# Kernel tuning notes

Measured on AMD Instinct MI355X. Metric: run time of the kernel, lower is better.

Reference implementation:

```python
import jax, jax.numpy as jnp
import numpy as np

B, S, D_IN, D_OUT, H = 2, 2048, 1024, 1024, 16
HD = D_OUT // H  # 64


def setup_inputs() -> dict:
    key = jax.random.key(0)
    ks = jax.random.split(key, 6)
    s = 0.02
    return {
        "x": jax.random.normal(ks[0], (B, S, D_IN), dtype=jnp.float32),
        "W_q": jax.random.normal(ks[1], (D_IN, D_OUT), dtype=jnp.float32) * s,
        "W_k": jax.random.normal(ks[2], (D_IN, D_OUT), dtype=jnp.float32) * s,
        "W_v": jax.random.normal(ks[3], (D_IN, D_OUT), dtype=jnp.float32) * s,
        "W_o": jax.random.normal(ks[4], (D_OUT, D_OUT), dtype=jnp.float32) * s,
        "b_o": jax.random.normal(ks[5], (D_OUT,), dtype=jnp.float32) * s,
    }


def reference(x, W_q, W_k, W_v, W_o, b_o):
    b, n, _ = x.shape
    # project and split heads: [b, h, n, hd]
    q = (x @ W_q).reshape(b, n, H, HD).transpose(0, 2, 1, 3)
    k = (x @ W_k).reshape(b, n, H, HD).transpose(0, 2, 1, 3)
    v = (x @ W_v).reshape(b, n, H, HD).transpose(0, 2, 1, 3)
    scores = jnp.einsum("bhqd,bhkd->bhqk", q, k) / jnp.sqrt(jnp.float32(HD))
    causal = jnp.tril(jnp.ones((n, n), dtype=bool))
    scores = jnp.where(causal, scores, -jnp.inf)
    attn = jax.nn.softmax(scores, axis=-1)  # dropout p=0.0 -> identity
    ctx = jnp.einsum("bhqk,bhkd->bhqd", attn, v)
    ctx = ctx.transpose(0, 2, 1, 3).reshape(b, n, D_OUT)
    return ctx @ W_o + b_o
```

## Files before the change

kernel.cpp:

```cpp
#include <hip/hip_runtime.h>

#define B_    2
#define S_    2048
#define DIN   1024
#define DOUT  1024
#define H_    16
#define HD_   64
#define M_    (B_ * S_)

typedef __bf16 bf16x8 __attribute__((ext_vector_type(8)));
typedef float  f32x4  __attribute__((ext_vector_type(4)));

__device__ __forceinline__ f32x4 MFMA(bf16x8 a, bf16x8 b, f32x4 c) {
    return __builtin_amdgcn_mfma_f32_16x16x32_bf16(a, b, c, 0, 0, 0);
}

__device__ __forceinline__ unsigned short f2b(float f) {
    union { float f; unsigned int u; } v; v.f = f;
    unsigned int u = v.u;
    return (unsigned short)((u + 0x7fffu + ((u >> 16) & 1u)) >> 16);
}

__device__ __forceinline__ unsigned pack2(float a, float b) {
    union { __bf16 h[2]; unsigned u; } cv;
    cv.h[0] = (__bf16)a; cv.h[1] = (__bf16)b;
    return cv.u;
}

#define GLDS(gp, lp) __builtin_amdgcn_global_load_lds( \
    (const __attribute__((address_space(1))) void*)(gp), \
    (__attribute__((address_space(3))) void*)(lp), 16, 0, 0)

#define QSCALE 0.1803368801111204f

__global__ __launch_bounds__(256) void k_cvt_all(const float* __restrict__ x,
                                                 const float* __restrict__ Wq,
                                                 const float* __restrict__ Wk,
                                                 const float* __restrict__ Wv,
                                                 const float* __restrict__ Wo,
                                                 unsigned short* __restrict__ xb,
                                                 unsigned short* __restrict__ WqkvT,
                                                 unsigned short* __restrict__ WoT) {
    __shared__ __align__(16) float tile[64][68];
    int bid = blockIdx.x;
    int tid = threadIdx.x;
    if (bid < 1024) {
#pragma unroll
        for (int j = 0; j < 4; j++) {
            int i = bid * 4096 + j * 1024 + tid * 4;
            float4 v = *reinterpret_cast<const float4*>(x + i);
            ushort4 o;
            o.x = f2b(v.x); o.y = f2b(v.y); o.z = f2b(v.z); o.w = f2b(v.w);
            *reinterpret_cast<ushort4*>(xb + i) = o;
        }
        return;
    }
    int wb = bid - 1024;
    int w = wb >> 8;
    int t = wb & 255;
    const float* src = (w == 0) ? Wq : (w == 1) ? Wk : (w == 2) ? Wv : Wo;
    unsigned short* dst = (w < 3) ? WqkvT + (size_t)w * 1024 * DIN : WoT;
    int k0 = (t >> 4) * 64, n0 = (t & 15) * 64;
#pragma unroll
    for (int j = 0; j < 4; j++) {
        int idx = j * 256 + tid;
        int r = idx >> 4, c4 = (idx & 15) * 4;
        *reinterpret_cast<float4*>(&tile[r][c4]) =
            *reinterpret_cast<const float4*>(&src[(size_t)(k0 + r) * DOUT + n0 + c4]);
    }
    __syncthreads();
#pragma unroll
    for (int j = 0; j < 2; j++) {
        int idx = j * 256 + tid;
        int n = idx >> 3, gk = (idx & 7) * 8;
        unsigned short o[8];
#pragma unroll
        for (int u = 0; u < 8; u++) o[u] = f2b(tile[gk + u][n]);
        *reinterpret_cast<int4*>(&dst[(size_t)(n0 + n) * DIN + k0 + gk]) =
            *reinterpret_cast<int4*>(o);
    }
}

__global__ __launch_bounds__(256) void k_trV(const unsigned short* __restrict__ V,
                                             unsigned short* __restrict__ Vt) {
    __shared__ unsigned short tile[64][72];
    int st = blockIdx.x, bh = blockIdx.y;
    int b = bh >> 4, h = bh & 15;
    int t = threadIdx.x;
    int r = t >> 2, c = (t & 3) << 4;
    const unsigned short* src = V + (size_t)(b * S_ + st * 64 + r) * DOUT + h * HD_ + c;
    *reinterpret_cast<int4*>(&tile[r][c])     = *reinterpret_cast<const int4*>(src);
    *reinterpret_cast<int4*>(&tile[r][c + 8]) = *reinterpret_cast<const int4*>(src + 8);
    __syncthreads();
    unsigned short o[16];
    for (int j = 0; j < 16; j++) o[j] = tile[c + j][r];
    unsigned short* dst = Vt + (size_t)(bh * 64 + r) * S_ + st * 64 + c;
    *reinterpret_cast<int4*>(dst)     = *reinterpret_cast<int4*>(&o[0]);
    *reinterpret_cast<int4*>(dst + 8) = *reinterpret_cast<int4*>(&o[8]);
}

template <int OUT_MODE, int BM>
__global__ __launch_bounds__(256) void k_gemm(const unsigned short* __restrict__ A,
                                              const unsigned short* __restrict__ Bt,
                                              unsigned short* __restrict__ Cq,
                                              unsigned short* __restrict__ Ck,
                                              unsigned short* __restrict__ Cv,
                                              float* __restrict__ Cf,
                                              const float* __restrict__ bias,
                                              int M, int N, int K, int nbx) {
    constexpr int MI = BM / 32;
    __shared__ __align__(16) unsigned short As[BM * 64];
    __shared__ __align__(16) unsigned short Bs[128 * 64];

    int nwg = gridDim.x;
    int chunkw = nwg >> 3;
    int bid = blockIdx.x;
    int nid = (bid & 7) * chunkw + (bid >> 3);
    int by = nid / nbx, bx = nid - by * nbx;
    int m0 = by * BM, n0 = bx * 128;

    int tid = threadIdx.x;
    int wid = tid >> 6, lane = tid & 63;
    int wm = wid >> 1, wn = wid & 1;
    int lr = lane & 15, lg = lane >> 4;

    f32x4 acc[MI][4] = {};

    int srow = lane >> 3;
    int scol = ((lane & 7) ^ srow) * 8;
    int rsw  = lr & 7;

    for (int k0 = 0; k0 < K; k0 += 64) {
#pragma unroll
        for (int c = 0; c < MI; c++) {
            int chunk = wid * MI + c;
            int row = chunk * 8 + srow;
            GLDS(A + (size_t)(m0 + row) * K + k0 + scol, (char*)As + chunk * 1024);
        }
#pragma unroll
        for (int c = 0; c < 4; c++) {
            int chunk = wid * 4 + c;
            int row = chunk * 8 + srow;
            GLDS(Bt + (size_t)(n0 + row) * K + k0 + scol, (char*)Bs + chunk * 1024);
        }
        __syncthreads();

#pragma unroll
        for (int kk = 0; kk < 2; kk++) {
            bf16x8 af[MI], bf[4];
#pragma unroll
            for (int mi = 0; mi < MI; mi++)
                af[mi] = *reinterpret_cast<const bf16x8*>(
                    &As[(wm * (BM / 2) + mi * 16 + lr) * 64 + (((kk * 4 + lg) ^ rsw) * 8)]);
#pragma unroll
            for (int ni = 0; ni < 4; ni++)
                bf[ni] = *reinterpret_cast<const bf16x8*>(
                    &Bs[(wn * 64 + ni * 16 + lr) * 64 + (((kk * 4 + lg) ^ rsw) * 8)]);
#pragma unroll
            for (int mi = 0; mi < MI; mi++)
#pragma unroll
                for (int ni = 0; ni < 4; ni++)
                    acc[mi][ni] = MFMA(af[mi], bf[ni], acc[mi][ni]);
        }
        __syncthreads();
    }

    for (int mi = 0; mi < MI; mi++)
        for (int ni = 0; ni < 4; ni++)
            for (int i = 0; i < 4; i++) {
                int row = m0 + wm * (BM / 2) + mi * 16 + lg * 4 + i;
                int col = n0 + wn * 64 + ni * 16 + lr;
                float v = acc[mi][ni][i];
                if (OUT_MODE == 2) {
                    Cf[(size_t)row * N + col] = v + bias[col];
                } else {
                    if (col < 1024)       Cq[(size_t)row * 1024 + col] = f2b(v * QSCALE);
                    else if (col < 2048)  Ck[(size_t)row * 1024 + (col - 1024)] = f2b(v);
                    else                  Cv[(size_t)row * 1024 + (col - 2048)] = f2b(v);
                }
            }
}

__global__ __launch_bounds__(512, 4) void k_attn(const unsigned short* __restrict__ Q,
                                                 const unsigned short* __restrict__ Kg,
                                                 const unsigned short* __restrict__ Vt,
                                                 unsigned short* __restrict__ ctx) {
    int p = blockIdx.x;
    int bh = blockIdx.y;
    int b = bh >> 4, h = bh & 15;
    int tid = threadIdx.x, wid = tid >> 6, lane = tid & 63;
    int lr = lane & 15, lg = lane >> 4;
    int qtB = 31 - p;
    int qt = (wid < 4) ? qtB : p;
    int q0 = qt * 64 + (wid & 3) * 16;

    __shared__ __align__(16) unsigned short Ks[4][64 * 64];
    __shared__ __align__(16) unsigned short Vs[4][64 * 64];
    __shared__ __align__(16) unsigned p_lds32[8][16 * 32];
    unsigned* pl32 = p_lds32[wid];

    const unsigned short* Qp = Q  + (size_t)b * S_ * DOUT + (size_t)h * HD_;
    const unsigned short* Kp = Kg + (size_t)b * S_ * DOUT + (size_t)h * HD_;
    const unsigned short* Vp = Vt + (size_t)(b * H_ + h) * HD_ * S_;

    bf16x8 qf0 = *reinterpret_cast<const bf16x8*>(&Qp[(size_t)(q0 + lr) * DOUT + lg * 8]);
    bf16x8 qf1 = *reinterpret_cast<const bf16x8*>(&Qp[(size_t)(q0 + lr) * DOUT + 32 + lg * 8]);
    asm volatile("" : "+v"(qf0), "+v"(qf1));

    int srow = lane >> 3;
    int scol = ((lane & 7) ^ srow) * 8;

#define STAGE_KV(buf, t)                                                           \
    {                                                                              \
        int kv0_ = (t) * 64;                                                       \
        int krow = wid * 8 + srow;                                                 \
        GLDS(Kp + (size_t)(kv0_ + krow) * DOUT + scol,                             \
             (char*)&Ks[buf][0] + wid * 1024);                                     \
        GLDS(Vp + (size_t)krow * S_ + kv0_ + scol,                                 \
             (char*)&Vs[buf][0] + wid * 1024);                                     \
    }

    int ntile = qtB + 1;
    STAGE_KV(0, 0)
    STAGE_KV(1, 1)

    f32x4 o[4] = {};
    float l = 0.f;
    int rxor = (lr & 7) << 4;
    int qg = q0 + lr;

    int cur = 0;
    for (int t = 0; t < ntile; t++) {
        int ahead = ntile - 1 - t;
        if (ahead >= 2) {
            STAGE_KV((cur + 2) & 3, t + 2)
            asm volatile("s_waitcnt vmcnt(4)" ::: "memory");
        } else if (ahead == 1) {
            asm volatile("s_waitcnt vmcnt(2)" ::: "memory");
        } else {
            asm volatile("s_waitcnt vmcnt(0)" ::: "memory");
        }
        __builtin_amdgcn_s_barrier();

        if (t <= qt) {
            const unsigned short* Kt = Ks[cur];
            const unsigned short* Vl = Vs[cur];
            int kv0 = t * 64;

            f32x4 s[4] = {};
            __builtin_amdgcn_s_setprio(1);
#pragma unroll
            for (int nf = 0; nf < 4; nf++)
#pragma unroll
                for (int kk = 0; kk < 2; kk++) {
                    bf16x8 kf = *reinterpret_cast<const bf16x8*>(
                        &Kt[(nf * 16 + lr) * 64 + (((kk * 64 + lg * 16) ^ rxor) >> 1)]);
                    s[nf] = MFMA(kf, kk ? qf1 : qf0, s[nf]);
                }
            __builtin_amdgcn_s_setprio(0);

            if (t == qt) {
#pragma unroll
                for (int nf = 0; nf < 4; nf++)
#pragma unroll
                    for (int i = 0; i < 4; i++)
                        if (kv0 + nf * 16 + lg * 4 + i > qg) s[nf][i] = -2000.0f;
            }

            f32x4 acc = {};
#pragma unroll
            for (int nf = 0; nf < 4; nf++) {
                f32x4 pv;
#pragma unroll
                for (int i = 0; i < 4; i++) pv[i] = exp2f(s[nf][i]);
                acc += pv;
                int unit = (nf * 2 + (lg >> 1)) ^ (lr & 7);
                uint2 wd; wd.x = pack2(pv[0], pv[1]); wd.y = pack2(pv[2], pv[3]);
                *reinterpret_cast<uint2*>(&pl32[lr * 32 + unit * 4 + (lg & 1) * 2]) = wd;
            }
            l += (acc[0] + acc[1]) + (acc[2] + acc[3]);

            bf16x8 pf[2];
#pragma unroll
            for (int kvb = 0; kvb < 2; kvb++)
                pf[kvb] = *reinterpret_cast<const bf16x8*>(
                    &pl32[lr * 32 + (((kvb * 4 + lg) ^ (lr & 7)) * 4)]);

            __builtin_amdgcn_s_setprio(1);
#pragma unroll
            for (int nd = 0; nd < 4; nd++)
#pragma unroll
                for (int kk = 0; kk < 2; kk++) {
                    bf16x8 vf = *reinterpret_cast<const bf16x8*>(
                        &Vl[(nd * 16 + lr) * 64 + (((kk * 64 + lg * 16) ^ rxor) >> 1)]);
                    o[nd] = MFMA(pf[kk], vf, o[nd]);
                }
            __builtin_amdgcn_s_setprio(0);
        }

        cur = (cur + 1) & 3;
    }

    l += __shfl_xor(l, 16, 64);
    l += __shfl_xor(l, 32, 64);

#pragma unroll
    for (int i = 0; i < 4; i++) {
        float li = __shfl(l, lg * 4 + i, 16);
        float r = __builtin_amdgcn_rcpf(li);
#pragma unroll
        for (int nd = 0; nd < 4; nd++)
            ((__bf16*)ctx)[((size_t)b * S_ + q0 + lg * 4 + i) * DOUT + h * HD_ + nd * 16 + lr] =
                (__bf16)(o[nd][i] * r);
    }
#undef STAGE_KV
}

extern "C" void kernel_launch(void* const* d_in, const int* in_sizes, int n_in,
                              void* d_out, int out_size, void* d_ws, size_t ws_size,
                              hipStream_t stream) {
    const float* x  = (const float*)d_in[0];
    const float* Wq = (const float*)d_in[1];
    const float* Wk = (const float*)d_in[2];
    const float* Wv = (const float*)d_in[3];
    const float* Wo = (const float*)d_in[4];
    const float* bo = (const float*)d_in[5];
    float* out = (float*)d_out;
    char* ws = (char*)d_ws;
    const size_t MB = 1u << 20;

    unsigned short* xb    = (unsigned short*)(ws);
    unsigned short* Vtb   = (unsigned short*)(ws);
    unsigned short* WqkvT = (unsigned short*)(ws + 8 * MB);
    unsigned short* WoT   = (unsigned short*)(ws + 14 * MB);
    unsigned short* Qb    = (unsigned short*)(ws + 16 * MB);
    unsigned short* Kb    = (unsigned short*)(ws + 24 * MB);
    unsigned short* Vb    = (unsigned short*)(ws + 32 * MB);
    unsigned short* ctx   = Vb;

    (void)in_sizes; (void)n_in; (void)out_size; (void)ws_size;

    k_cvt_all<<<2048, 256, 0, stream>>>(x, Wq, Wk, Wv, Wo, xb, WqkvT, WoT);

    k_gemm<0, 128><<<768, 256, 0, stream>>>(xb, WqkvT, Qb, Kb, Vb, nullptr, nullptr,
                                            M_, 3072, DIN, 24);

    dim3 gt(S_ / 64, B_ * H_);
    k_trV<<<gt, 256, 0, stream>>>(Vb, Vtb);

    dim3 ga(16, B_ * H_);
    k_attn<<<ga, 512, 0, stream>>>(Qb, Kb, Vtb, ctx);

    k_gemm<2, 64><<<512, 256, 0, stream>>>(ctx, WoT, nullptr, nullptr, nullptr,
                                           out, bo, M_, DOUT, DOUT, 8);
}
```

Before: 113.6 us.

## Fuse V transpose into QKV GEMM epilogue and double-buffer GEMM K-tiles

Removes the separate k_trV kernel: QKV GEMM blocks covering the V columns stage their bf16 tile transposed in LDS and write V^T directly in the layout attention expects. The GEMM main loop now uses K-steps of 32 with double-buffered LDS stages and a single barrier per step, so the loads for the next tile overlap the current MFMAs. The weight-conversion transpose tile also gets an XOR swizzle to avoid LDS bank conflicts. Workspace layout is reshuffled so ctx reuses the xb region. The cost is more loop iterations with smaller K-steps and extra epilogue LDS traffic for V blocks.

After: 106.3 us. 6.4% less time.

```diff
diff --git a/kernel.cpp b/kernel.cpp
--- a/kernel.cpp
+++ b/kernel.cpp
@@ -64,39 +64,26 @@
 #pragma unroll
     for (int j = 0; j < 4; j++) {
         int idx = j * 256 + tid;
-        int r = idx >> 4, c4 = (idx & 15) * 4;
-        *reinterpret_cast<float4*>(&tile[r][c4]) =
-            *reinterpret_cast<const float4*>(&src[(size_t)(k0 + r) * DOUT + n0 + c4]);
+        int r = idx >> 4, c4g = idx & 15;
+        int sg = c4g ^ ((r >> 3) & 7);
+        *reinterpret_cast<float4*>(&tile[r][sg * 4]) =
+            *reinterpret_cast<const float4*>(&src[(size_t)(k0 + r) * DOUT + n0 + c4g * 4]);
     }
     __syncthreads();
 #pragma unroll
     for (int j = 0; j < 2; j++) {
         int idx = j * 256 + tid;
         int n = idx >> 3, gk = (idx & 7) * 8;
+        int g = n >> 2, e = n & 3;
         unsigned short o[8];
 #pragma unroll
-        for (int u = 0; u < 8; u++) o[u] = f2b(tile[gk + u][n]);
+        for (int u = 0; u < 8; u++) {
+            int k = gk + u;
+            o[u] = f2b(tile[k][((g ^ ((k >> 3) & 7)) << 2) + e]);
+        }
         *reinterpret_cast<int4*>(&dst[(size_t)(n0 + n) * DIN + k0 + gk]) =
             *reinterpret_cast<int4*>(o);
     }
-}
-
-__global__ __launch_bounds__(256) void k_trV(const unsigned short* __restrict__ V,
-                                             unsigned short* __restrict__ Vt) {
-    __shared__ unsigned short tile[64][72];
-    int st = blockIdx.x, bh = blockIdx.y;
-    int b = bh >> 4, h = bh & 15;
-    int t = threadIdx.x;
-    int r = t >> 2, c = (t & 3) << 4;
-    const unsigned short* src = V + (size_t)(b * S_ + st * 64 + r) * DOUT + h * HD_ + c;
-    *reinterpret_cast<int4*>(&tile[r][c])     = *reinterpret_cast<const int4*>(src);
-    *reinterpret_cast<int4*>(&tile[r][c + 8]) = *reinterpret_cast<const int4*>(src + 8);
-    __syncthreads();
-    unsigned short o[16];
-    for (int j = 0; j < 16; j++) o[j] = tile[c + j][r];
-    unsigned short* dst = Vt + (size_t)(bh * 64 + r) * S_ + st * 64 + c;
-    *reinterpret_cast<int4*>(dst)     = *reinterpret_cast<int4*>(&o[0]);
-    *reinterpret_cast<int4*>(dst + 8) = *reinterpret_cast<int4*>(&o[8]);
 }
 
 template <int OUT_MODE, int BM>
@@ -104,13 +91,17 @@
                                               const unsigned short* __restrict__ Bt,
                                               unsigned short* __restrict__ Cq,
                                               unsigned short* __restrict__ Ck,
-                                              unsigned short* __restrict__ Cv,
+                                              unsigned short* __restrict__ Cvt,
                                               float* __restrict__ Cf,
                                               const float* __restrict__ bias,
                                               int M, int N, int K, int nbx) {
-    constexpr int MI = BM / 32;
-    __shared__ __align__(16) unsigned short As[BM * 64];
-    __shared__ __align__(16) unsigned short Bs[128 * 64];
+    constexpr int MI  = BM / 32;
+    constexpr int ASZ = BM * 32;
+    constexpr int BSZ = 128 * 32;
+    constexpr int ACH = BM / 64;
+    constexpr int STG = 2 * (ASZ + BSZ);
+    constexpr int SMEM_N = (OUT_MODE == 0 && STG < 17408) ? 17408 : STG;
+    __shared__ __align__(16) unsigned short smem[SMEM_N];
 
     int nwg = gridDim.x;
     int chunkw = nwg >> 3;
@@ -126,59 +117,104 @@
 
     f32x4 acc[MI][4] = {};
 
-    int srow = lane >> 3;
-    int scol = ((lane & 7) ^ srow) * 8;
-    int rsw  = lr & 7;
-
-    for (int k0 = 0; k0 < K; k0 += 64) {
-#pragma unroll
-        for (int c = 0; c < MI; c++) {
-            int chunk = wid * MI + c;
-            int row = chunk * 8 + srow;
-            GLDS(A + (size_t)(m0 + row) * K + k0 + scol, (char*)As + chunk * 1024);
-        }
-#pragma unroll
-        for (int c = 0; c < 4; c++) {
-            int chunk = wid * 4 + c;
-            int row = chunk * 8 + srow;
-            GLDS(Bt + (size_t)(n0 + row) * K + k0 + scol, (char*)Bs + chunk * 1024);
-        }
+    int srow = lane >> 2;
+    int scol = ((lane & 3) ^ (srow & 3)) * 8;
+    int runit = (lg ^ (lr & 3)) * 8;
+
+#define STAGE_G(buf, k0)                                                       \
+    {                                                                          \
+        unsigned short* Ad = smem + (buf) * ASZ;                               \
+        unsigned short* Bd = smem + 2 * ASZ + (buf) * BSZ;                     \
+        _Pragma("unroll")                                                      \
+        for (int c = 0; c < ACH; c++) {                                        \
+            int chunk = wid * ACH + c;                                         \
+            int row = chunk * 16 + srow;                                       \
+            GLDS(A + (size_t)(m0 + row) * K + (k0) + scol,                     \
+                 (char*)Ad + chunk * 1024);                                    \
+        }                                                                      \
+        _Pragma("unroll")                                                      \
+        for (int c = 0; c < 2; c++) {                                          \
+            int chunk = wid * 2 + c;                                           \
+            int row = chunk * 16 + srow;                                       \
+            GLDS(Bt + (size_t)(n0 + row) * K + (k0) + scol,                    \
+                 (char*)Bd + chunk * 1024);                                    \
+        }                                                                      \
+    }
+
+    STAGE_G(0, 0)
+    __syncthreads();
+
+    int nkt = K >> 5;
+    for (int kt = 0; kt < nkt; kt++) {
+        int buf = kt & 1;
+        if (kt + 1 < nkt) STAGE_G(buf ^ 1, (kt + 1) * 32)
+
+        const unsigned short* Asr = smem + buf * ASZ;
+        const unsigned short* Bsr = smem + 2 * ASZ + buf * BSZ;
+        bf16x8 af[MI], bf[4];
+#pragma unroll
+        for (int mi = 0; mi < MI; mi++)
+            af[mi] = *reinterpret_cast<const bf16x8*>(
+                &Asr[(wm * (BM / 2) + mi * 16 + lr) * 32 + runit]);
+#pragma unroll
+        for (int ni = 0; ni < 4; ni++)
+            bf[ni] = *reinterpret_cast<const bf16x8*>(
+                &Bsr[(wn * 64 + ni * 16 + lr) * 32 + runit]);
+#pragma unroll
+        for (int mi = 0; mi < MI; mi++)
+#pragma unroll
+            for (int ni = 0; ni < 4; ni++)
+                acc[mi][ni] = MFMA(af[mi], bf[ni], acc[mi][ni]);
+
+        asm volatile("s_waitcnt vmcnt(0)" ::: "memory");
+        __builtin_amdgcn_s_barrier();
+    }
+
+    if (OUT_MODE == 2) {
+        for (int mi = 0; mi < MI; mi++)
+            for (int ni = 0; ni < 4; ni++)
+                for (int i = 0; i < 4; i++) {
+                    int row = m0 + wm * (BM / 2) + mi * 16 + lg * 4 + i;
+                    int col = n0 + wn * 64 + ni * 16 + lr;
+                    Cf[(size_t)row * N + col] = acc[mi][ni][i] + bias[col];
+                }
+    } else if (n0 < 2048) {
+        unsigned short* Cd = (n0 < 1024) ? Cq : Ck;
+        int cb = (n0 < 1024) ? 0 : 1024;
+        float sc = (n0 < 1024) ? QSCALE : 1.0f;
+        for (int mi = 0; mi < MI; mi++)
+            for (int ni = 0; ni < 4; ni++)
+                for (int i = 0; i < 4; i++) {
+                    int row = m0 + wm * (BM / 2) + mi * 16 + lg * 4 + i;
+                    int col = n0 + wn * 64 + ni * 16 + lr;
+                    Cd[(size_t)row * 1024 + (col - cb)] = f2b(acc[mi][ni][i] * sc);
+                }
+    } else {
+        unsigned short* Lt = smem;
+        for (int mi = 0; mi < MI; mi++)
+            for (int ni = 0; ni < 4; ni++) {
+                int cl = wn * 64 + ni * 16 + lr;
+                int rl0 = wm * (BM / 2) + mi * 16 + lg * 4;
+                uint2 wd;
+                wd.x = pack2(acc[mi][ni][0], acc[mi][ni][1]);
+                wd.y = pack2(acc[mi][ni][2], acc[mi][ni][3]);
+                *reinterpret_cast<uint2*>(&Lt[cl * 136 + rl0]) = wd;
+            }
         __syncthreads();
-
-#pragma unroll
-        for (int kk = 0; kk < 2; kk++) {
-            bf16x8 af[MI], bf[4];
-#pragma unroll
-            for (int mi = 0; mi < MI; mi++)
-                af[mi] = *reinterpret_cast<const bf16x8*>(
-                    &As[(wm * (BM / 2) + mi * 16 + lr) * 64 + (((kk * 4 + lg) ^ rsw) * 8)]);
-#pragma unroll
-            for (int ni = 0; ni < 4; ni++)
-                bf[ni] = *reinterpret_cast<const bf16x8*>(
-                    &Bs[(wn * 64 + ni * 16 + lr) * 64 + (((kk * 4 + lg) ^ rsw) * 8)]);
-#pragma unroll
-            for (int mi = 0; mi < MI; mi++)
-#pragma unroll
-                for (int ni = 0; ni < 4; ni++)
-                    acc[mi][ni] = MFMA(af[mi], bf[ni], acc[mi][ni]);
-        }
-        __syncthreads();
-    }
-
-    for (int mi = 0; mi < MI; mi++)
-        for (int ni = 0; ni < 4; ni++)
-            for (int i = 0; i < 4; i++) {
-                int row = m0 + wm * (BM / 2) + mi * 16 + lg * 4 + i;
-                int col = n0 + wn * 64 + ni * 16 + lr;
-                float v = acc[mi][ni][i];
-                if (OUT_MODE == 2) {
-                    Cf[(size_t)row * N + col] = v + bias[col];
-                } else {
-                    if (col < 1024)       Cq[(size_t)row * 1024 + col] = f2b(v * QSCALE);
-                    else if (col < 2048)  Ck[(size_t)row * 1024 + (col - 1024)] = f2b(v);
-                    else                  Cv[(size_t)row * 1024 + (col - 2048)] = f2b(v);
-                }
-            }
+        int b = m0 >> 11, ms = m0 & (S_ - 1);
+        int bh64 = (b * H_ + ((n0 - 2048) >> 6)) * 64;
+#pragma unroll
+        for (int it = 0; it < 4; it++) {
+            int cl = it * 32 + (tid >> 3);
+            int ss = (tid & 7) * 16;
+            int4 v0 = *reinterpret_cast<int4*>(&Lt[cl * 136 + ss]);
+            int4 v1 = *reinterpret_cast<int4*>(&Lt[cl * 136 + ss + 8]);
+            unsigned short* dp = Cvt + (size_t)(bh64 + cl) * S_ + ms + ss;
+            *reinterpret_cast<int4*>(dp) = v0;
+            *reinterpret_cast<int4*>(dp + 8) = v1;
+        }
+    }
+#undef STAGE_G
 }
 
 __global__ __launch_bounds__(512, 4) void k_attn(const unsigned short* __restrict__ Q,
@@ -330,23 +366,19 @@
     const size_t MB = 1u << 20;
 
     unsigned short* xb    = (unsigned short*)(ws);
-    unsigned short* Vtb   = (unsigned short*)(ws);
+    unsigned short* ctx   = (unsigned short*)(ws);
     unsigned short* WqkvT = (unsigned short*)(ws + 8 * MB);
     unsigned short* WoT   = (unsigned short*)(ws + 14 * MB);
     unsigned short* Qb    = (unsigned short*)(ws + 16 * MB);
     unsigned short* Kb    = (unsigned short*)(ws + 24 * MB);
-    unsigned short* Vb    = (unsigned short*)(ws + 32 * MB);
-    unsigned short* ctx   = Vb;
+    unsigned short* Vtb   = (unsigned short*)(ws + 32 * MB);
 
     (void)in_sizes; (void)n_in; (void)out_size; (void)ws_size;
 
     k_cvt_all<<<2048, 256, 0, stream>>>(x, Wq, Wk, Wv, Wo, xb, WqkvT, WoT);
 
-    k_gemm<0, 128><<<768, 256, 0, stream>>>(xb, WqkvT, Qb, Kb, Vb, nullptr, nullptr,
+    k_gemm<0, 128><<<768, 256, 0, stream>>>(xb, WqkvT, Qb, Kb, Vtb, nullptr, nullptr,
                                             M_, 3072, DIN, 24);
-
-    dim3 gt(S_ / 64, B_ * H_);
-    k_trV<<<gt, 256, 0, stream>>>(Vb, Vtb);
 
     dim3 ga(16, B_ * H_);
     k_attn<<<ga, 512, 0, stream>>>(Qb, Kb, Vtb, ctx);
```
